# Kernel optimization log

Measured on AMD Instinct MI355X. Metric: run time of the kernel, lower is better.

The kernel has to match this reference:

```python
import jax, jax.numpy as jnp
import numpy as np

D_MODEL = 1024
N_HEADS = 16
HEAD_DIM = D_MODEL // N_HEADS


def setup_inputs() -> dict:
    key = jax.random.key(0)
    ks = jax.random.split(key, 5)
    B, T = 2, 2048
    x = jax.random.normal(ks[0], (B, T, D_MODEL), dtype=jnp.float32)
    s = 1.0 / np.sqrt(D_MODEL)
    qkv_w = jax.random.uniform(ks[1], (3 * D_MODEL, D_MODEL), jnp.float32, -s, s)
    qkv_b = jax.random.uniform(ks[2], (3 * D_MODEL,), jnp.float32, -s, s)
    out_w = jax.random.uniform(ks[3], (D_MODEL, D_MODEL), jnp.float32, -s, s)
    out_b = jax.random.uniform(ks[4], (D_MODEL,), jnp.float32, -s, s)
    return {"x": x, "qkv_w": qkv_w, "qkv_b": qkv_b, "out_w": out_w, "out_b": out_b}


def reference(x, qkv_w, qkv_b, out_w, out_b):
    B, T, _ = x.shape
    # qkv projection: [B,T,3*D]
    qkv = x @ qkv_w.T + qkv_b
    qkv = qkv.reshape(B, T, 3, N_HEADS, HEAD_DIM)
    qkv = jnp.transpose(qkv, (2, 0, 3, 1, 4))  # [3,B,H,T,Hd]
    q, k, v = qkv[0], qkv[1], qkv[2]
    scale = 1.0 / np.sqrt(HEAD_DIM)
    scores = jnp.einsum("bhqd,bhkd->bhqk", q, k) * scale  # [B,H,T,T]
    causal = jnp.tril(jnp.ones((T, T), dtype=bool))
    scores = jnp.where(causal, scores, -jnp.inf)
    weights = jax.nn.softmax(scores, axis=-1)
    # dropout in eval mode (identity)
    out = jnp.einsum("bhqk,bhkd->bhqd", weights, v)  # [B,H,T,Hd]
    out = jnp.transpose(out, (0, 2, 1, 3)).reshape(B, T, D_MODEL)
    return out @ out_w.T + out_b
```

## Files before the change

### kernel.cpp

```cpp
#include <hip/hip_runtime.h>
#include <hip/hip_bf16.h>


typedef __bf16 bf16;
typedef bf16 bf16x8 __attribute__((ext_vector_type(8)));
typedef bf16 bf16x4 __attribute__((ext_vector_type(4)));
typedef float f32x4 __attribute__((ext_vector_type(4)));

#define MFMA16(a, b, c) __builtin_amdgcn_mfma_f32_16x16x32_bf16((a), (b), (c), 0, 0, 0)

static constexpr int D_MODEL = 1024;
static constexpr int NH = 16;
static constexpr int HD = 64;
static constexpr int SEQ = 2048;
static constexpr int NB = 2;
static constexpr float QSCALE = 0.125f * 1.44269504088896340736f;

__device__ __forceinline__ bf16x8 cvt8(const float* p) {
    float4 u0 = *(const float4*)p;
    float4 u1 = *(const float4*)(p + 4);
    bf16x8 v = { (bf16)u0.x, (bf16)u0.y, (bf16)u0.z, (bf16)u0.w,
                 (bf16)u1.x, (bf16)u1.y, (bf16)u1.z, (bf16)u1.w };
    return v;
}

__device__ __forceinline__ void async16(const bf16* g, bf16* l) {
    __builtin_amdgcn_global_load_lds(
        (const __attribute__((address_space(1))) void*)g,
        (__attribute__((address_space(3))) void*)l, 16, 0, 0);
}

static constexpr int X8 = 524288;
static constexpr int W8 = 917504;
static constexpr int T8 = 1048576;

__global__ __launch_bounds__(256)
void k_cast_all(const float* __restrict__ x, const float* __restrict__ qkv_w,
                const float* __restrict__ out_w,
                bf16* __restrict__ xb, bf16* __restrict__ wqb,
                bf16* __restrict__ wob)
{
    int i = blockIdx.x * 256 + threadIdx.x;
    if (i < X8) {
        *(bf16x8*)&xb[(size_t)i * 8] = cvt8(&x[(size_t)i * 8]);
    } else if (i < W8) {
        int j = i - X8;
        *(bf16x8*)&wqb[(size_t)j * 8] = cvt8(&qkv_w[(size_t)j * 8]);
    } else if (i < T8) {
        int j = i - W8;
        *(bf16x8*)&wob[(size_t)j * 8] = cvt8(&out_w[(size_t)j * 8]);
    }
}

__global__ __launch_bounds__(256)
void k_qkv(const bf16* __restrict__ x, const bf16* __restrict__ w,
           const float* __restrict__ bias,
           bf16* __restrict__ Qb, bf16* __restrict__ Kb, bf16* __restrict__ VbT)
{
    __shared__ bf16 As[128 * 32];
    __shared__ bf16 Ws[128 * 32];

    const int tid  = threadIdx.x;
    const int wv   = tid >> 6;
    const int lane = tid & 63;
    const int lr   = lane & 15;
    const int lk   = lane >> 4;
    const int wm   = wv >> 1, wn = wv & 1;
    const int m0   = blockIdx.x * 128;
    const int n0   = blockIdx.y * 128;

    const int sRow = tid >> 2;
    const int sCol = (tid & 3) * 8;
    const int sOff = sRow * 32 + sCol;

    f32x4 acc[4][4] = {};

    for (int kt = 0; kt < 1024; kt += 32) {
        __syncthreads();
        async16(&x[(size_t)(m0 + sRow     ) * 1024 + kt + sCol], &As[sOff]);
        async16(&x[(size_t)(m0 + 64 + sRow) * 1024 + kt + sCol], &As[64 * 32 + sOff]);
        async16(&w[(size_t)(n0 + sRow     ) * 1024 + kt + sCol], &Ws[sOff]);
        async16(&w[(size_t)(n0 + 64 + sRow) * 1024 + kt + sCol], &Ws[64 * 32 + sOff]);
        __syncthreads();

        bf16x8 a[4], b[4];
        #pragma unroll
        for (int i = 0; i < 4; i++) {
            a[i] = *(const bf16x8*)&As[(wm * 64 + i * 16 + lr) * 32 + lk * 8];
            b[i] = *(const bf16x8*)&Ws[(wn * 64 + i * 16 + lr) * 32 + lk * 8];
        }
        #pragma unroll
        for (int i = 0; i < 4; i++)
            #pragma unroll
            for (int j = 0; j < 4; j++)
                acc[i][j] = MFMA16(a[i], b[j], acc[i][j]);
    }

    #pragma unroll
    for (int i = 0; i < 4; i++) {
        #pragma unroll
        for (int j = 0; j < 4; j++) {
            const int gm0 = m0 + wm * 64 + i * 16 + lk * 4;
            const int gn  = n0 + wn * 64 + j * 16 + lr;
            const int sel = gn >> 10;
            const int rem = gn & 1023;
            const int h   = rem >> 6;
            const int hd  = rem & 63;
            const int bb  = gm0 >> 11;
            const int t0  = gm0 & 2047;
            if (sel == 2) {
                bf16x4 p;
                #pragma unroll
                for (int r = 0; r < 4; r++) p[r] = (bf16)(acc[i][j][r] + bias[gn]);
                *(bf16x4*)&VbT[((size_t)(bb * NH + h) * HD + hd) * SEQ + t0] = p;
            } else {
                #pragma unroll
                for (int r = 0; r < 4; r++) {
                    float v = acc[i][j][r] + bias[gn];
                    size_t idx = ((size_t)(bb * NH + h) * SEQ + t0 + r) * HD + hd;
                    if (sel == 0) Qb[idx] = (bf16)(v * QSCALE);
                    else          Kb[idx] = (bf16)v;
                }
            }
        }
    }
}

__global__ __launch_bounds__(256)
void k_attn(const bf16* __restrict__ Qb, const bf16* __restrict__ Kb,
            const bf16* __restrict__ VbT, bf16* __restrict__ AO)
{
    __shared__ bf16 Ks[2][64 * 64];
    __shared__ bf16 Vt[2][64 * 64];
    __shared__ bf16 Ps[64 * 64];

    const int tid  = threadIdx.x;
    const int wv   = tid >> 6;
    const int lane = tid & 63;
    const int lr   = lane & 15;
    const int lk   = lane >> 4;
    const int bh   = blockIdx.y;
    const int qt   = ((bh >> 3) & 1) ? (31 - (int)blockIdx.x) : (int)blockIdx.x;

    const bf16* Qp  = Qb  + (size_t)bh * SEQ * HD;
    const bf16* Kp  = Kb  + (size_t)bh * SEQ * HD;
    const bf16* Vtp = VbT + (size_t)bh * HD * SEQ;

    const int qg = qt * 64 + wv * 16 + lr;

    bf16x8 qf[2];
    qf[0] = *(const bf16x8*)&Qp[(size_t)qg * HD +      lk * 8];
    qf[1] = *(const bf16x8*)&Qp[(size_t)qg * HD + 32 + lk * 8];

    f32x4 ot[4] = {};
    float lsum = 0.f;

    const int srow   = tid >> 3;
    const int sgcol  = ((tid & 7) ^ (srow & 7)) * 8;
    const int sldse  = tid * 8;
    const int swz    = lr & 7;

    auto stage = [&](int buf, int k0) {
        async16(&Kp [(size_t)(k0 + srow     ) * HD  + sgcol], &Ks[buf][       sldse]);
        async16(&Kp [(size_t)(k0 + 32 + srow) * HD  + sgcol], &Ks[buf][2048 + sldse]);
        async16(&Vtp[(size_t)(srow          ) * SEQ + k0 + sgcol], &Vt[buf][       sldse]);
        async16(&Vtp[(size_t)(32 + srow     ) * SEQ + k0 + sgcol], &Vt[buf][2048 + sldse]);
    };

    stage(0, 0);

    for (int kt = 0; kt <= qt; kt++) {
        const int p = kt & 1;
        if (kt < qt) {
            stage(p ^ 1, (kt + 1) * 64);
            asm volatile("s_waitcnt vmcnt(4)" ::: "memory");
        } else {
            asm volatile("s_waitcnt vmcnt(0)" ::: "memory");
        }
        __builtin_amdgcn_s_barrier();

        f32x4 s[4] = {};
        #pragma unroll
        for (int j = 0; j < 4; j++) {
            #pragma unroll
            for (int c = 0; c < 2; c++) {
                bf16x8 ka = *(const bf16x8*)
                    &Ks[p][(j * 16 + lr) * 64 + (((4 * c + lk) ^ swz) << 3)];
                s[j] = MFMA16(ka, qf[c], s[j]);
            }
        }

        const int k0 = kt * 64;
        const bool diag = (kt == qt);
        #pragma unroll
        for (int j = 0; j < 4; j++) {
            const int keyb = k0 + j * 16 + lk * 4;
            f32x4 pv;
            #pragma unroll
            for (int r = 0; r < 4; r++) {
                float e = __builtin_amdgcn_exp2f(s[j][r]);
                if (diag) e = (keyb + r > qg) ? 0.f : e;
                pv[r] = e;
            }
            s[j] = pv;
            lsum += (pv[0] + pv[1]) + (pv[2] + pv[3]);
        }

        #pragma unroll
        for (int j = 0; j < 4; j++) {
            bf16x4 p4 = { (bf16)s[j][0], (bf16)s[j][1], (bf16)s[j][2], (bf16)s[j][3] };
            *(bf16x4*)&Ps[(wv * 16 + lr) * 64 +
                          (((2 * j + (lk >> 1)) ^ swz) << 3) + ((lk & 1) << 2)] = p4;
        }

        #pragma unroll
        for (int c = 0; c < 2; c++) {
            bf16x8 pb = *(const bf16x8*)
                &Ps[(wv * 16 + lr) * 64 + (((4 * c + lk) ^ swz) << 3)];
            #pragma unroll
            for (int jh = 0; jh < 4; jh++) {
                bf16x8 va = *(const bf16x8*)
                    &Vt[p][(jh * 16 + lr) * 64 + (((4 * c + lk) ^ swz) << 3)];
                ot[jh] = MFMA16(va, pb, ot[jh]);
            }
        }

        asm volatile("" ::: "memory");
        __builtin_amdgcn_s_barrier();
    }

    lsum += __shfl_xor(lsum, 16);
    lsum += __shfl_xor(lsum, 32);

    const float inv = 1.0f / lsum;
    const int b_ = bh >> 4, h_ = bh & 15;
    const size_t base = ((size_t)(b_ * SEQ + qg)) * D_MODEL + h_ * HD;
    #pragma unroll
    for (int jh = 0; jh < 4; jh++) {
        bf16x4 o4 = { (bf16)(ot[jh][0] * inv), (bf16)(ot[jh][1] * inv),
                      (bf16)(ot[jh][2] * inv), (bf16)(ot[jh][3] * inv) };
        *(bf16x4*)&AO[base + jh * 16 + lk * 4] = o4;
    }
}

__global__ __launch_bounds__(256)
void k_oproj(const bf16* __restrict__ a_, const bf16* __restrict__ w,
             const float* __restrict__ bias, float* __restrict__ out)
{
    __shared__ bf16 As[128 * 32];
    __shared__ bf16 Ws[64 * 32];

    const int tid  = threadIdx.x;
    const int wv   = tid >> 6;
    const int lane = tid & 63;
    const int lr   = lane & 15;
    const int lk   = lane >> 4;
    const int wm   = wv >> 1, wn = wv & 1;
    const int m0   = blockIdx.x * 128;
    const int n0   = blockIdx.y * 64;

    const int sRow = tid >> 2;
    const int sCol = (tid & 3) * 8;
    const int sOff = sRow * 32 + sCol;

    f32x4 acc[4][2] = {};

    for (int kt = 0; kt < 1024; kt += 32) {
        __syncthreads();
        async16(&a_[(size_t)(m0 + sRow     ) * 1024 + kt + sCol], &As[sOff]);
        async16(&a_[(size_t)(m0 + 64 + sRow) * 1024 + kt + sCol], &As[64 * 32 + sOff]);
        async16(&w [(size_t)(n0 + sRow     ) * 1024 + kt + sCol], &Ws[sOff]);
        __syncthreads();

        bf16x8 a[4], b[2];
        #pragma unroll
        for (int i = 0; i < 4; i++)
            a[i] = *(const bf16x8*)&As[(wm * 64 + i * 16 + lr) * 32 + lk * 8];
        #pragma unroll
        for (int j = 0; j < 2; j++)
            b[j] = *(const bf16x8*)&Ws[(wn * 32 + j * 16 + lr) * 32 + lk * 8];
        #pragma unroll
        for (int i = 0; i < 4; i++)
            #pragma unroll
            for (int j = 0; j < 2; j++)
                acc[i][j] = MFMA16(a[i], b[j], acc[i][j]);
    }

    #pragma unroll
    for (int i = 0; i < 4; i++) {
        #pragma unroll
        for (int j = 0; j < 2; j++) {
            #pragma unroll
            for (int r = 0; r < 4; r++) {
                int gm = m0 + wm * 64 + i * 16 + lk * 4 + r;
                int gn = n0 + wn * 32 + j * 16 + lr;
                out[(size_t)gm * 1024 + gn] = acc[i][j][r] + bias[gn];
            }
        }
    }
}

extern "C" void kernel_launch(void* const* d_in, const int* in_sizes, int n_in,
                              void* d_out, int out_size, void* d_ws, size_t ws_size,
                              hipStream_t stream)
{
    const float* x     = (const float*)d_in[0];
    const float* qkv_w = (const float*)d_in[1];
    const float* qkv_b = (const float*)d_in[2];
    const float* out_w = (const float*)d_in[3];
    const float* out_b = (const float*)d_in[4];
    float* out = (float*)d_out;

    const size_t SZ = (size_t)NB * NH * SEQ * HD;
    bf16* Qb  = (bf16*)d_ws;
    bf16* Kb  = Qb + SZ;
    bf16* VbT = Kb + SZ;
    bf16* AO  = VbT + SZ;
    bf16* xb  = AO + SZ;
    bf16* wqb = xb + SZ;
    bf16* wob = wqb + (size_t)3 * D_MODEL * D_MODEL;

    hipLaunchKernelGGL(k_cast_all, dim3(4096), dim3(256), 0, stream,
                       x, qkv_w, out_w, xb, wqb, wob);

    hipLaunchKernelGGL(k_qkv, dim3(32, 24), dim3(256), 0, stream,
                       xb, wqb, qkv_b, Qb, Kb, VbT);
    hipLaunchKernelGGL(k_attn, dim3(32, 32), dim3(256), 0, stream,
                       Qb, Kb, VbT, AO);
    hipLaunchKernelGGL(k_oproj, dim3(32, 16), dim3(256), 0, stream,
                       AO, wob, out_b, out);
}
```

Before: 171.5 us.

## Rewrite QKV GEMM as 256x256 double-buffered tile with swizzled LDS

The QKV projection GEMM moves from 128x128 tiles with 256 threads and single-buffered K=32 steps to 256x256 tiles with 512 threads. It uses K=64 steps, double-buffered dynamic LDS (128 KB), an XOR swizzle against bank conflicts, and prefetch of the next tile overlapped with MFMA work under raised wave priority. The aim is more data reuse per loaded byte and hiding global load latency. The trade-off is only 192 blocks for the GPU's CUs, so occupancy is lower and there may be tail imbalance, plus a large LDS footprint and register pressure from 32 accumulators per lane.

```diff
diff --git a/kernel.cpp b/kernel.cpp
--- a/kernel.cpp
+++ b/kernel.cpp
@@ -52,56 +52,92 @@
     }
 }
 
-__global__ __launch_bounds__(256)
+__global__ __launch_bounds__(512)
 void k_qkv(const bf16* __restrict__ x, const bf16* __restrict__ w,
            const float* __restrict__ bias,
            bf16* __restrict__ Qb, bf16* __restrict__ Kb, bf16* __restrict__ VbT)
 {
-    __shared__ bf16 As[128 * 32];
-    __shared__ bf16 Ws[128 * 32];
+    extern __shared__ bf16 Sdyn[];
 
     const int tid  = threadIdx.x;
-    const int wv   = tid >> 6;
+    const int wid  = tid >> 6;
     const int lane = tid & 63;
     const int lr   = lane & 15;
     const int lk   = lane >> 4;
-    const int wm   = wv >> 1, wn = wv & 1;
-    const int m0   = blockIdx.x * 128;
-    const int n0   = blockIdx.y * 128;
-
-    const int sRow = tid >> 2;
-    const int sCol = (tid & 3) * 8;
-    const int sOff = sRow * 32 + sCol;
-
-    f32x4 acc[4][4] = {};
-
-    for (int kt = 0; kt < 1024; kt += 32) {
-        __syncthreads();
-        async16(&x[(size_t)(m0 + sRow     ) * 1024 + kt + sCol], &As[sOff]);
-        async16(&x[(size_t)(m0 + 64 + sRow) * 1024 + kt + sCol], &As[64 * 32 + sOff]);
-        async16(&w[(size_t)(n0 + sRow     ) * 1024 + kt + sCol], &Ws[sOff]);
-        async16(&w[(size_t)(n0 + 64 + sRow) * 1024 + kt + sCol], &Ws[64 * 32 + sOff]);
-        __syncthreads();
-
-        bf16x8 a[4], b[4];
-        #pragma unroll
-        for (int i = 0; i < 4; i++) {
-            a[i] = *(const bf16x8*)&As[(wm * 64 + i * 16 + lr) * 32 + lk * 8];
-            b[i] = *(const bf16x8*)&Ws[(wn * 64 + i * 16 + lr) * 32 + lk * 8];
-        }
-        #pragma unroll
-        for (int i = 0; i < 4; i++)
-            #pragma unroll
-            for (int j = 0; j < 4; j++)
-                acc[i][j] = MFMA16(a[i], b[j], acc[i][j]);
-    }
+    const int wr   = wid >> 2;
+    const int wc   = wid & 3;
+    const int m0   = blockIdx.x * 256;
+    const int n0   = blockIdx.y * 256;
+
+    const int srow   = tid >> 3;
+    const int schunk = (tid & 7) ^ (srow & 7);
+    const int sldse  = tid * 8;
+    const int swz    = lr & 7;
+
+    auto piece = [&](int buf, int tensor, int half) -> bf16* {
+        return Sdyn + (((buf * 2 + tensor) * 2 + half) * 8192);
+    };
+
+    auto stageHalf = [&](int buf, int tensor, int hsub, int kt) {
+        const bf16* gp   = tensor ? w : x;
+        const int  grow0 = (tensor ? n0 : m0) + hsub * 128;
+        bf16* lbase = piece(buf, tensor, hsub);
+        #pragma unroll
+        for (int l = 0; l < 2; l++) {
+            async16(&gp[(size_t)(grow0 + l * 64 + srow) * 1024 + kt + schunk * 8],
+                    &lbase[l * 4096 + sldse]);
+        }
+    };
+
+    f32x4 acc[8][4] = {};
 
     #pragma unroll
-    for (int i = 0; i < 4; i++) {
+    for (int q = 0; q < 4; q++) stageHalf(0, q >> 1, q & 1, 0);
+    asm volatile("s_waitcnt vmcnt(0)" ::: "memory");
+    __builtin_amdgcn_s_barrier();
+
+    for (int T = 0; T < 16; T++) {
+        const int buf = T & 1;
+        bf16x8 bfr[4];
+        #pragma unroll
+        for (int p = 0; p < 4; p++) {
+            const int kh = p >> 1, ms = p & 1;
+            bf16x8 af[4];
+            #pragma unroll
+            for (int i = 0; i < 4; i++)
+                af[i] = *(const bf16x8*)&piece(buf, 0, wr)
+                        [(ms * 64 + i * 16 + lr) * 64 + (((kh * 4 + lk) ^ swz) << 3)];
+            if (ms == 0) {
+                #pragma unroll
+                for (int j = 0; j < 4; j++)
+                    bfr[j] = *(const bf16x8*)&piece(buf, 1, wc >> 1)
+                        [((wc & 1) * 64 + j * 16 + lr) * 64 + (((kh * 4 + lk) ^ swz) << 3)];
+            }
+            if (p == 0 && T < 15) {
+                #pragma unroll
+                for (int q = 0; q < 4; q++) stageHalf(buf ^ 1, q >> 1, q & 1, (T + 1) * 64);
+            }
+            __builtin_amdgcn_s_barrier();
+            __builtin_amdgcn_s_setprio(1);
+            #pragma unroll
+            for (int i = 0; i < 4; i++)
+                #pragma unroll
+                for (int j = 0; j < 4; j++)
+                    acc[ms * 4 + i][j] = MFMA16(af[i], bfr[j], acc[ms * 4 + i][j]);
+            __builtin_amdgcn_s_setprio(0);
+            if (p == 3) asm volatile("s_waitcnt vmcnt(0)" ::: "memory");
+            asm volatile("" ::: "memory");
+            __builtin_amdgcn_s_barrier();
+        }
+    }
+
+    #pragma unroll
+    for (int a = 0; a < 8; a++) {
+        const int ms = a >> 2, i = a & 3;
         #pragma unroll
         for (int j = 0; j < 4; j++) {
-            const int gm0 = m0 + wm * 64 + i * 16 + lk * 4;
-            const int gn  = n0 + wn * 64 + j * 16 + lr;
+            const int gm0 = m0 + wr * 128 + ms * 64 + i * 16 + lk * 4;
+            const int gn  = n0 + wc * 64 + j * 16 + lr;
             const int sel = gn >> 10;
             const int rem = gn & 1023;
             const int h   = rem >> 6;
@@ -109,14 +145,14 @@
             const int bb  = gm0 >> 11;
             const int t0  = gm0 & 2047;
             if (sel == 2) {
-                bf16x4 p;
-                #pragma unroll
-                for (int r = 0; r < 4; r++) p[r] = (bf16)(acc[i][j][r] + bias[gn]);
-                *(bf16x4*)&VbT[((size_t)(bb * NH + h) * HD + hd) * SEQ + t0] = p;
+                bf16x4 pv;
+                #pragma unroll
+                for (int r = 0; r < 4; r++) pv[r] = (bf16)(acc[a][j][r] + bias[gn]);
+                *(bf16x4*)&VbT[((size_t)(bb * NH + h) * HD + hd) * SEQ + t0] = pv;
             } else {
                 #pragma unroll
                 for (int r = 0; r < 4; r++) {
-                    float v = acc[i][j][r] + bias[gn];
+                    float v = acc[a][j][r] + bias[gn];
                     size_t idx = ((size_t)(bb * NH + h) * SEQ + t0 + r) * HD + hd;
                     if (sel == 0) Qb[idx] = (bf16)(v * QSCALE);
                     else          Kb[idx] = (bf16)v;
@@ -323,7 +359,7 @@
     hipLaunchKernelGGL(k_cast_all, dim3(4096), dim3(256), 0, stream,
                        x, qkv_w, out_w, xb, wqb, wob);
 
-    hipLaunchKernelGGL(k_qkv, dim3(32, 24), dim3(256), 0, stream,
+    hipLaunchKernelGGL(k_qkv, dim3(16, 12), dim3(512), 131072, stream,
                        xb, wqb, qkv_b, Qb, Kb, VbT);
     hipLaunchKernelGGL(k_attn, dim3(32, 32), dim3(256), 0, stream,
                        Qb, Kb, VbT, AO);
```

Measured after the change: 178.2 us. 3.9% more time.
